# Kernel optimization log

Hardware: AMD Instinct MI355X
Metric: run time of the kernel (lower is better)

## Reference

```python
import jax, jax.numpy as jnp
import numpy as np

N_USERS = 100000
N_ITEMS = 50000
EMB_DIM = 64
N_LAYERS = 2
N_INTENTS = 128
N_EDGES = 4000000
N_NODES = N_USERS + N_ITEMS


def setup_inputs() -> dict:
    key = jax.random.key(0)
    k1, k2, k3, k4, k5 = jax.random.split(key, 5)
    return {
        "user_emb": 0.1 * jax.random.normal(k1, (N_USERS, EMB_DIM), dtype=jnp.float32),
        "item_emb": 0.1 * jax.random.normal(k2, (N_ITEMS, EMB_DIM), dtype=jnp.float32),
        "intents": jax.random.normal(k3, (EMB_DIM, N_INTENTS), dtype=jnp.float32) * (2.0 / (EMB_DIM + N_INTENTS)) ** 0.5,
        "h_idx": jax.random.randint(k4, (N_EDGES,), 0, N_NODES, dtype=jnp.int64)
        if jax.config.jax_enable_x64 else jax.random.randint(k4, (N_EDGES,), 0, N_NODES, dtype=jnp.int32),
        "t_idx": jax.random.randint(k5, (N_EDGES,), 0, N_NODES, dtype=jnp.int32),
    }


def _spmm(h_idx, t_idx, g_vals, x):
    # y[h] += g_vals * x[t]  (sparse matrix @ dense, COO form)
    gathered = x[t_idx] * g_vals[:, None]  # [E, D]
    return jax.ops.segment_sum(gathered, h_idx, num_segments=N_NODES)


def reference(user_emb, item_emb, intents, h_idx, t_idx):
    # --- _cal_sparse_adj: G = D^{-1/2} A D^{-1/2}, A values are ones ---
    deg = jax.ops.segment_sum(jnp.ones_like(h_idx, dtype=user_emb.dtype), h_idx,
                              num_segments=N_NODES)
    d_inv_sqrt = jnp.where(deg > 0, jax.lax.rsqrt(jnp.maximum(deg, 1e-12)), 0.0)
    g_vals = d_inv_sqrt[h_idx] * d_inv_sqrt[t_idx]  # [E]

    # --- multi-layer propagation with intent-aware embeddings ---
    embs = jnp.concatenate([user_emb, item_emb], axis=0)  # [N, D]
    all_embs = [embs]
    for _ in range(N_LAYERS):
        gnn_embs = _spmm(h_idx, t_idx, g_vals, embs)  # [N, D]
        # intent projection: softmax over intents, reconstruct in emb space
        u, it = embs[:N_USERS], embs[N_USERS:]
        u_int = jax.nn.softmax(u @ intents, axis=1) @ intents.T      # [n_users, D]
        i_int = jax.nn.softmax(it @ intents, axis=1) @ intents.T     # [n_items, D]
        int_embs = jnp.concatenate([u_int, i_int], axis=0)
        embs = gnn_embs + int_embs
        all_embs.append(embs)
    out = jnp.sum(jnp.stack(all_embs, axis=1), axis=1) / len(all_embs)  # mean over layers
    return out
```

## Files before the change

kernel.cpp:

```cpp
#include <hip/hip_runtime.h>
#include <math.h>

#define N_USERS 100000
#define N_ITEMS 50000
#define N_NODES 150000
#define EMB 64
#define NI 128
#define NUM_EDGES 4000000
#define NPAD 150016
#define NB 586
#define BSTRIDE 8192
#define ETILE 8192
#define EGRID ((NUM_EDGES + ETILE - 1) / ETILE)
#define NTILES (N_NODES / 16)
#define SBLK ((NTILES + 3) / 4)

typedef __attribute__((ext_vector_type(8))) short bf16x8;
typedef __attribute__((ext_vector_type(4))) float f32x4;

__device__ __forceinline__ unsigned short f2bf(float f) {
    unsigned int u = __float_as_uint(f);
    u += 0x7FFFu + ((u >> 16) & 1u);
    return (unsigned short)(u >> 16);
}
__device__ __forceinline__ float bflo(unsigned int u) { return __uint_as_float(u << 16); }
__device__ __forceinline__ float bfhi(unsigned int u) { return __uint_as_float(u & 0xFFFF0000u); }
__device__ __forceinline__ int cl_idx(unsigned int v) {
    int x = (int)(v & 0x3FFFFu);
    return (x < N_NODES) ? x : (N_NODES - 1);
}


__global__ __launch_bounds__(512) void bucket_scatter(const int* __restrict__ h,
                                                      const int* __restrict__ t,
                                                      int* __restrict__ gcur,
                                                      unsigned int* __restrict__ ebuf) {
    __shared__ int lc[NB];
    __shared__ int lbase[NB];
    __shared__ int lcur[NB];
    int tid = threadIdx.x;
    for (int i = tid; i < NB; i += 512) lc[i] = 0;
    __syncthreads();
    int base = blockIdx.x * ETILE;
#pragma unroll
    for (int k = 0; k < ETILE / 512; ++k) {
        int idx = base + k * 512 + tid;
        if (idx < NUM_EDGES) atomicAdd(&lc[h[idx] >> 8], 1);
    }
    __syncthreads();
    for (int i = tid; i < NB; i += 512) {
        int c = lc[i];
        lbase[i] = c ? (i * BSTRIDE + atomicAdd(&gcur[i], c)) : 0;
        lcur[i] = 0;
    }
    __syncthreads();
#pragma unroll
    for (int k = 0; k < ETILE / 512; ++k) {
        int idx = base + k * 512 + tid;
        if (idx < NUM_EDGES) {
            int hh = h[idx], tt = t[idx];
            int b = hh >> 8;
            int p = lbase[b] + atomicAdd(&lcur[b], 1);
            int lim = b * BSTRIDE + BSTRIDE - 1;
            p = (p <= lim) ? p : lim;
            ebuf[p] = ((unsigned int)(hh & 255) << 18) | (unsigned int)tt;
        }
    }
}


__global__ __launch_bounds__(512) void bucket_csr(const int* __restrict__ gcur,
                                                  unsigned int* __restrict__ ebuf,
                                                  int2* __restrict__ rmeta,
                                                  float* __restrict__ dinv) {
    __shared__ unsigned int in_s[BSTRIDE];
    __shared__ int cnt_s[256];
    __shared__ int base_s[256];
    __shared__ int sc[256];
    int b = blockIdx.x, tid = threadIdx.x;
    int s = b * BSTRIDE;
    int n = gcur[b];
    if (n > BSTRIDE) n = BSTRIDE;

    for (int i = tid; i < n; i += 512) in_s[i] = ebuf[s + i];
    if (tid < 256) cnt_s[tid] = 0;
    __syncthreads();
    for (int i = tid; i < n; i += 512) atomicAdd(&cnt_s[in_s[i] >> 18], 1);
    __syncthreads();

    int c = 0;
    if (tid < 256) { c = cnt_s[tid]; sc[tid] = c; }
    __syncthreads();
    for (int off = 1; off < 256; off <<= 1) {
        int tv = 0;
        if (tid < 256 && tid >= off) tv = sc[tid - off];
        __syncthreads();
        if (tid < 256 && tid >= off) sc[tid] += tv;
        __syncthreads();
    }
    if (tid < 256) {
        int excl = sc[tid] - c;
        base_s[tid] = excl;
        int node = (b << 8) + tid;
        rmeta[node] = make_int2(s + excl, c);
        dinv[node] = (c > 0) ? rsqrtf((float)c) : 0.0f;
        cnt_s[tid] = 0;
    }
    __syncthreads();

    for (int i = tid; i < n; i += 512) {
        unsigned int qv = in_s[i];
        int hl = (int)(qv >> 18);
        int p = base_s[hl] + atomicAdd(&cnt_s[hl], 1);
        ebuf[s + p] = qv & 0x3FFFFu;
    }
}


__global__ void init_kernel(const float4* __restrict__ ue4, const float4* __restrict__ ie4,
                            uint2* __restrict__ ebf4, float4* __restrict__ out4) {
    int i = blockIdx.x * blockDim.x + threadIdx.x;
    const int uelems = N_USERS * EMB / 4;
    const int total  = N_NODES * EMB / 4;
    if (i < total) {
        float4 v = (i < uelems) ? ue4[i] : ie4[i - uelems];
        out4[i] = v;
        unsigned int p0 = ((unsigned int)f2bf(v.y) << 16) | f2bf(v.x);
        unsigned int p1 = ((unsigned int)f2bf(v.w) << 16) | f2bf(v.z);
        ebf4[i] = make_uint2(p0, p1);
    }
}


__global__ __launch_bounds__(256) void wconv(const float* __restrict__ W,
                                             unsigned short* __restrict__ Wt,
                                             unsigned short* __restrict__ W2b) {
    int i = blockIdx.x * 256 + threadIdx.x;
    if (i < EMB * NI) {
        int d = i >> 7, c = i & 127;
        unsigned short b = f2bf(W[i]);
        W2b[i] = b;
        Wt[c * EMB + d] = b;
    }
}


__global__ __launch_bounds__(256, 6) void spmm_intent(const int2* __restrict__ rmeta,
                                                      const unsigned int* __restrict__ col,
                                                      const float* __restrict__ dinv,
                                                      const unsigned short* __restrict__ ebf,
                                                      unsigned short* __restrict__ ebfout,
                                                      const unsigned short* __restrict__ Wt,
                                                      const unsigned short* __restrict__ W2b,
                                                      float* __restrict__ acc, float scale) {
    __shared__ __align__(16) float UPool[4][1408];

    int tid = threadIdx.x;
    int wid = tid >> 6, lane = tid & 63;
    int q = lane >> 4, c = lane & 15;
    int qq = lane >> 3, cc = lane & 7;
    int tile = blockIdx.x * 4 + wid;
    if (tile >= NTILES) return;
    int rowbase = tile << 4;
    float* fw = &UPool[wid][0];
    unsigned short* pw = (unsigned short*)&UPool[wid][1088];

#pragma unroll 1
    for (int half = 0; half < 2; ++half) {
        int row = rowbase + half * 8 + qq;
        int2 rm = rmeta[row];
        int s = rm.x, deg = rm.y;
        float dr = dinv[row];
        int dm = deg;
        dm = max(dm, __shfl_xor(dm, 8));
        dm = max(dm, __shfl_xor(dm, 16));
        dm = max(dm, __shfl_xor(dm, 32));
        dm = __builtin_amdgcn_readfirstlane(dm);

        float a0 = 0.f, a1 = 0.f, a2 = 0.f, a3 = 0.f;
        float a4 = 0.f, a5 = 0.f, a6 = 0.f, a7 = 0.f;
        int last = s + ((deg > 0) ? (deg - 1) : 0);
        const unsigned short* eb = ebf + (cc << 3);

        int ce0 = cl_idx(col[s]);
        int ce1 = cl_idx(col[min(s + 1, last)]);
        int ce2 = cl_idx(col[min(s + 2, last)]);
        int ce3 = cl_idx(col[min(s + 3, last)]);
        float g0 = dinv[ce0], g1 = dinv[ce1], g2 = dinv[ce2], g3 = dinv[ce3];
        uint4 u0 = *(const uint4*)(eb + ((size_t)ce0 << 6));
        uint4 u1 = *(const uint4*)(eb + ((size_t)ce1 << 6));
        uint4 u2 = *(const uint4*)(eb + ((size_t)ce2 << 6));
        uint4 u3 = *(const uint4*)(eb + ((size_t)ce3 << 6));
        int nc0 = cl_idx(col[min(s + 4, last)]);
        int nc1 = cl_idx(col[min(s + 5, last)]);
        int nc2 = cl_idx(col[min(s + 6, last)]);
        int nc3 = cl_idx(col[min(s + 7, last)]);

        for (int it = 0; it < dm; it += 4) {
            int f0 = cl_idx(col[min(s + it + 8, last)]);
            int f1 = cl_idx(col[min(s + it + 9, last)]);
            int f2 = cl_idx(col[min(s + it + 10, last)]);
            int f3 = cl_idx(col[min(s + it + 11, last)]);
            float h0 = dinv[nc0], h1 = dinv[nc1], h2 = dinv[nc2], h3 = dinv[nc3];
            uint4 v0 = *(const uint4*)(eb + ((size_t)nc0 << 6));
            uint4 v1 = *(const uint4*)(eb + ((size_t)nc1 << 6));
            uint4 v2 = *(const uint4*)(eb + ((size_t)nc2 << 6));
            uint4 v3 = *(const uint4*)(eb + ((size_t)nc3 << 6));
            float gu0 = (it     < deg) ? g0 : 0.f;
            float gu1 = (it + 1 < deg) ? g1 : 0.f;
            float gu2 = (it + 2 < deg) ? g2 : 0.f;
            float gu3 = (it + 3 < deg) ? g3 : 0.f;
            a0 = fmaf(gu0, bflo(u0.x), a0); a1 = fmaf(gu0, bfhi(u0.x), a1);
            a2 = fmaf(gu0, bflo(u0.y), a2); a3 = fmaf(gu0, bfhi(u0.y), a3);
            a4 = fmaf(gu0, bflo(u0.z), a4); a5 = fmaf(gu0, bfhi(u0.z), a5);
            a6 = fmaf(gu0, bflo(u0.w), a6); a7 = fmaf(gu0, bfhi(u0.w), a7);
            a0 = fmaf(gu1, bflo(u1.x), a0); a1 = fmaf(gu1, bfhi(u1.x), a1);
            a2 = fmaf(gu1, bflo(u1.y), a2); a3 = fmaf(gu1, bfhi(u1.y), a3);
            a4 = fmaf(gu1, bflo(u1.z), a4); a5 = fmaf(gu1, bfhi(u1.z), a5);
            a6 = fmaf(gu1, bflo(u1.w), a6); a7 = fmaf(gu1, bfhi(u1.w), a7);
            a0 = fmaf(gu2, bflo(u2.x), a0); a1 = fmaf(gu2, bfhi(u2.x), a1);
            a2 = fmaf(gu2, bflo(u2.y), a2); a3 = fmaf(gu2, bfhi(u2.y), a3);
            a4 = fmaf(gu2, bflo(u2.z), a4); a5 = fmaf(gu2, bfhi(u2.z), a5);
            a6 = fmaf(gu2, bflo(u2.w), a6); a7 = fmaf(gu2, bfhi(u2.w), a7);
            a0 = fmaf(gu3, bflo(u3.x), a0); a1 = fmaf(gu3, bfhi(u3.x), a1);
            a2 = fmaf(gu3, bflo(u3.y), a2); a3 = fmaf(gu3, bfhi(u3.y), a3);
            a4 = fmaf(gu3, bflo(u3.z), a4); a5 = fmaf(gu3, bfhi(u3.z), a5);
            a6 = fmaf(gu3, bflo(u3.w), a6); a7 = fmaf(gu3, bfhi(u3.w), a7);
            u0 = v0; u1 = v1; u2 = v2; u3 = v3;
            g0 = h0; g1 = h1; g2 = h2; g3 = h3;
            nc0 = f0; nc1 = f1; nc2 = f2; nc3 = f3;
        }
        int fb = (half * 8 + qq) * 68 + (cc << 3);
        fw[fb + 0] = a0 * dr; fw[fb + 1] = a1 * dr;
        fw[fb + 2] = a2 * dr; fw[fb + 3] = a3 * dr;
        fw[fb + 4] = a4 * dr; fw[fb + 5] = a5 * dr;
        fw[fb + 6] = a6 * dr; fw[fb + 7] = a7 * dr;
    }

    const unsigned short* erow = ebf + ((size_t)(rowbase + c) << 6);
    bf16x8 A0 = *(const bf16x8*)(erow + (q << 3));
    bf16x8 A1 = *(const bf16x8*)(erow + 32 + (q << 3));
    f32x4 S[8];
#pragma unroll
    for (int t = 0; t < 8; ++t) {
        bf16x8 B0 = *(const bf16x8*)&Wt[(16 * t + c) * EMB + (q << 3)];
        bf16x8 B1 = *(const bf16x8*)&Wt[(16 * t + c) * EMB + 32 + (q << 3)];
        f32x4 z = {0.f, 0.f, 0.f, 0.f};
        z = __builtin_amdgcn_mfma_f32_16x16x32_bf16(A0, B0, z, 0, 0, 0);
        S[t] = __builtin_amdgcn_mfma_f32_16x16x32_bf16(A1, B1, z, 0, 0, 0);
    }

#pragma unroll
    for (int r = 0; r < 4; ++r) {
        float m = S[0][r];
#pragma unroll
        for (int t = 1; t < 8; ++t) m = fmaxf(m, S[t][r]);
        m = fmaxf(m, __shfl_xor(m, 1)); m = fmaxf(m, __shfl_xor(m, 2));
        m = fmaxf(m, __shfl_xor(m, 4)); m = fmaxf(m, __shfl_xor(m, 8));
        float sum = 0.f;
#pragma unroll
        for (int t = 0; t < 8; ++t) { float ex = __expf(S[t][r] - m); S[t][r] = ex; sum += ex; }
        sum += __shfl_xor(sum, 1); sum += __shfl_xor(sum, 2);
        sum += __shfl_xor(sum, 4); sum += __shfl_xor(sum, 8);
        float inv = 1.0f / sum;
#pragma unroll
        for (int t = 0; t < 8; ++t) S[t][r] *= inv;
    }

    f32x4 O0 = {0.f, 0.f, 0.f, 0.f}, O1 = O0, O2 = O0, O3 = O0;
#pragma unroll
    for (int s2 = 0; s2 < 4; ++s2) {
#pragma unroll
        for (int h2 = 0; h2 < 2; ++h2) {
            int t = 2 * s2 + h2;
#pragma unroll
            for (int r = 0; r < 4; ++r) {
                float p = S[t][r];
                unsigned short b = f2bf(p);
                pw[(4 * q + r) * 40 + (h2 << 4) + c] = b;
                S[t][r] = p - bflo((unsigned int)b);
            }
        }
        bf16x8 Pf = *(const bf16x8*)&pw[c * 40 + (q << 3)];
        {
            bf16x8 Bf0 = *(const bf16x8*)&W2b[(c) * NI + (s2 << 5) + (q << 3)];
            bf16x8 Bf1 = *(const bf16x8*)&W2b[(16 + c) * NI + (s2 << 5) + (q << 3)];
            O0 = __builtin_amdgcn_mfma_f32_16x16x32_bf16(Pf, Bf0, O0, 0, 0, 0);
            O1 = __builtin_amdgcn_mfma_f32_16x16x32_bf16(Pf, Bf1, O1, 0, 0, 0);
            bf16x8 Bf2 = *(const bf16x8*)&W2b[(32 + c) * NI + (s2 << 5) + (q << 3)];
            bf16x8 Bf3 = *(const bf16x8*)&W2b[(48 + c) * NI + (s2 << 5) + (q << 3)];
            O2 = __builtin_amdgcn_mfma_f32_16x16x32_bf16(Pf, Bf2, O2, 0, 0, 0);
            O3 = __builtin_amdgcn_mfma_f32_16x16x32_bf16(Pf, Bf3, O3, 0, 0, 0);
        }
#pragma unroll
        for (int h2 = 0; h2 < 2; ++h2) {
            int t = 2 * s2 + h2;
#pragma unroll
            for (int r = 0; r < 4; ++r)
                pw[(4 * q + r) * 40 + (h2 << 4) + c] = f2bf(S[t][r]);
        }
        bf16x8 Pl = *(const bf16x8*)&pw[c * 40 + (q << 3)];
        {
            bf16x8 Bf0 = *(const bf16x8*)&W2b[(c) * NI + (s2 << 5) + (q << 3)];
            bf16x8 Bf1 = *(const bf16x8*)&W2b[(16 + c) * NI + (s2 << 5) + (q << 3)];
            O0 = __builtin_amdgcn_mfma_f32_16x16x32_bf16(Pl, Bf0, O0, 0, 0, 0);
            O1 = __builtin_amdgcn_mfma_f32_16x16x32_bf16(Pl, Bf1, O1, 0, 0, 0);
            bf16x8 Bf2 = *(const bf16x8*)&W2b[(32 + c) * NI + (s2 << 5) + (q << 3)];
            bf16x8 Bf3 = *(const bf16x8*)&W2b[(48 + c) * NI + (s2 << 5) + (q << 3)];
            O2 = __builtin_amdgcn_mfma_f32_16x16x32_bf16(Pl, Bf2, O2, 0, 0, 0);
            O3 = __builtin_amdgcn_mfma_f32_16x16x32_bf16(Pl, Bf3, O3, 0, 0, 0);
        }
    }

    asm volatile("" ::: "memory");

#pragma unroll
    for (int r = 0; r < 4; ++r) {
        int rl = 4 * q + r;
        float* gr = &fw[rl * 68];
        gr[c]      += O0[r];
        gr[16 + c] += O1[r];
        gr[32 + c] += O2[r];
        gr[48 + c] += O3[r];
    }

    {
        int j = lane >> 2, sg = lane & 3;
        const float* gr = &fw[j * 68 + (sg << 4)];
        float4 x0 = *(const float4*)&gr[0];
        float4 x1 = *(const float4*)&gr[4];
        float4 x2 = *(const float4*)&gr[8];
        float4 x3 = *(const float4*)&gr[12];
        size_t base = ((size_t)(rowbase + j) << 6) + (sg << 4);
        uint4 w0, w1;
        w0.x = (unsigned int)f2bf(x0.x) | ((unsigned int)f2bf(x0.y) << 16);
        w0.y = (unsigned int)f2bf(x0.z) | ((unsigned int)f2bf(x0.w) << 16);
        w0.z = (unsigned int)f2bf(x1.x) | ((unsigned int)f2bf(x1.y) << 16);
        w0.w = (unsigned int)f2bf(x1.z) | ((unsigned int)f2bf(x1.w) << 16);
        w1.x = (unsigned int)f2bf(x2.x) | ((unsigned int)f2bf(x2.y) << 16);
        w1.y = (unsigned int)f2bf(x2.z) | ((unsigned int)f2bf(x2.w) << 16);
        w1.z = (unsigned int)f2bf(x3.x) | ((unsigned int)f2bf(x3.y) << 16);
        w1.w = (unsigned int)f2bf(x3.z) | ((unsigned int)f2bf(x3.w) << 16);
        *(uint4*)(ebfout + base) = w0;
        *(uint4*)(ebfout + base + 8) = w1;
        float4* ap = (float4*)(acc + base);
        float4 b0 = ap[0], b1 = ap[1], b2 = ap[2], b3 = ap[3];
        b0.x = (b0.x + x0.x) * scale; b0.y = (b0.y + x0.y) * scale;
        b0.z = (b0.z + x0.z) * scale; b0.w = (b0.w + x0.w) * scale;
        b1.x = (b1.x + x1.x) * scale; b1.y = (b1.y + x1.y) * scale;
        b1.z = (b1.z + x1.z) * scale; b1.w = (b1.w + x1.w) * scale;
        b2.x = (b2.x + x2.x) * scale; b2.y = (b2.y + x2.y) * scale;
        b2.z = (b2.z + x2.z) * scale; b2.w = (b2.w + x2.w) * scale;
        b3.x = (b3.x + x3.x) * scale; b3.y = (b3.y + x3.y) * scale;
        b3.z = (b3.z + x3.z) * scale; b3.w = (b3.w + x3.w) * scale;
        ap[0] = b0; ap[1] = b1; ap[2] = b2; ap[3] = b3;
    }
}


extern "C" void kernel_launch(void* const* d_in, const int* in_sizes, int n_in,
                              void* d_out, int out_size, void* d_ws, size_t ws_size,
                              hipStream_t stream) {
    const float* ue = (const float*)d_in[0];
    const float* ie = (const float*)d_in[1];
    const float* W  = (const float*)d_in[2];
    const int*   h  = (const int*)d_in[3];
    const int*   t  = (const int*)d_in[4];
    float* out = (float*)d_out;

    int*            gcur  = (int*)d_ws;
    int2*           rmeta = (int2*)(gcur + 1024);
    float*          dinv  = (float*)(rmeta + NPAD);
    unsigned int*   ebuf  = (unsigned int*)(dinv + NPAD);
    unsigned short* Wt    = (unsigned short*)(ebuf + NB * BSTRIDE);
    unsigned short* W2b   = Wt + EMB * NI;
    unsigned short* ebfA  = W2b + EMB * NI;
    unsigned short* ebfB  = ebfA + (size_t)NPAD * EMB;

    hipMemsetAsync(gcur, 0, NB * sizeof(int), stream);
    bucket_scatter<<<EGRID, 512, 0, stream>>>(h, t, gcur, ebuf);
    bucket_csr<<<NB, 512, 0, stream>>>(gcur, ebuf, rmeta, dinv);
    init_kernel<<<(N_NODES * EMB / 4 + 255) / 256, 256, 0, stream>>>(
        (const float4*)ue, (const float4*)ie, (uint2*)ebfA, (float4*)out);
    wconv<<<(EMB * NI + 255) / 256, 256, 0, stream>>>(W, Wt, W2b);

    const unsigned int* col = ebuf;
    spmm_intent<<<SBLK, 256, 0, stream>>>(rmeta, col, dinv, ebfA, ebfB, Wt, W2b, out, 1.0f);
    spmm_intent<<<SBLK, 256, 0, stream>>>(rmeta, col, dinv, ebfB, ebfA, Wt, W2b, out, 1.0f / 3.0f);
}
```

Before: 453.2 us.

## Sort rows by degree within buckets and pad row lengths with sentinel edges

The CSR build now pads each row's edge list to a multiple of four using a sentinel column that points at a zeroed padding node, and it produces a per-bucket permutation that orders nodes by descending degree. The SpMM kernel processes rows in permuted order, so the eight rows sharing a wavefront have similar degrees. This removes the per-edge bounds clamps, the degree masks and the wavefront max-degree reduction. Occupancy hint raised from 6 to 7. Risks: a bucket can overflow BSTRIDE once padding is added, and rows are written in scattered permuted order.

```diff
diff --git a/kernel.cpp b/kernel.cpp
--- a/kernel.cpp
+++ b/kernel.cpp
@@ -12,8 +12,9 @@
 #define BSTRIDE 8192
 #define ETILE 8192
 #define EGRID ((NUM_EDGES + ETILE - 1) / ETILE)
-#define NTILES (N_NODES / 16)
-#define SBLK ((NTILES + 3) / 4)
+#define NT_ALL (NPAD / 16)
+#define SBLK (NT_ALL / 4)
+#define SENT 150000u
 
 typedef __attribute__((ext_vector_type(8))) short bf16x8;
 typedef __attribute__((ext_vector_type(4))) float f32x4;
@@ -25,10 +26,6 @@
 }
 __device__ __forceinline__ float bflo(unsigned int u) { return __uint_as_float(u << 16); }
 __device__ __forceinline__ float bfhi(unsigned int u) { return __uint_as_float(u & 0xFFFF0000u); }
-__device__ __forceinline__ int cl_idx(unsigned int v) {
-    int x = (int)(v & 0x3FFFFu);
-    return (x < N_NODES) ? x : (N_NODES - 1);
-}
 
 
 __global__ __launch_bounds__(512) void bucket_scatter(const int* __restrict__ h,
@@ -72,24 +69,33 @@
 __global__ __launch_bounds__(512) void bucket_csr(const int* __restrict__ gcur,
                                                   unsigned int* __restrict__ ebuf,
                                                   int2* __restrict__ rmeta,
-                                                  float* __restrict__ dinv) {
+                                                  float* __restrict__ dinv,
+                                                  int* __restrict__ perm) {
     __shared__ unsigned int in_s[BSTRIDE];
     __shared__ int cnt_s[256];
     __shared__ int base_s[256];
     __shared__ int sc[256];
+    __shared__ int dh[256];
+    __shared__ int dcur[256];
     int b = blockIdx.x, tid = threadIdx.x;
     int s = b * BSTRIDE;
     int n = gcur[b];
     if (n > BSTRIDE) n = BSTRIDE;
 
     for (int i = tid; i < n; i += 512) in_s[i] = ebuf[s + i];
-    if (tid < 256) cnt_s[tid] = 0;
+    if (tid < 256) { cnt_s[tid] = 0; dh[tid] = 0; dcur[tid] = 0; }
     __syncthreads();
     for (int i = tid; i < n; i += 512) atomicAdd(&cnt_s[in_s[i] >> 18], 1);
     __syncthreads();
 
-    int c = 0;
-    if (tid < 256) { c = cnt_s[tid]; sc[tid] = c; }
+    int c = 0, pc = 0, key = 0;
+    if (tid < 256) {
+        c = cnt_s[tid];
+        pc = (c + 3) & ~3;
+        sc[tid] = pc;
+        key = 255 - min(c, 255);
+        atomicAdd(&dh[key], 1);
+    }
     __syncthreads();
     for (int off = 1; off < 256; off <<= 1) {
         int tv = 0;
@@ -98,16 +104,28 @@
         if (tid < 256 && tid >= off) sc[tid] += tv;
         __syncthreads();
     }
+    int excl = 0;
+    if (tid < 256) { excl = sc[tid] - pc; base_s[tid] = excl; }
+    __syncthreads();
+    if (tid < 256) sc[tid] = dh[tid];
+    __syncthreads();
+    for (int off = 1; off < 256; off <<= 1) {
+        int tv = 0;
+        if (tid < 256 && tid >= off) tv = sc[tid - off];
+        __syncthreads();
+        if (tid < 256 && tid >= off) sc[tid] += tv;
+        __syncthreads();
+    }
     if (tid < 256) {
-        int excl = sc[tid] - c;
-        base_s[tid] = excl;
         int node = (b << 8) + tid;
-        rmeta[node] = make_int2(s + excl, c);
+        rmeta[node] = make_int2(s + excl, pc);
         dinv[node] = (c > 0) ? rsqrtf((float)c) : 0.0f;
+        int pos = (sc[key] - dh[key]) + atomicAdd(&dcur[key], 1);
+        perm[(b << 8) + pos] = node;
+        for (int p2 = c; p2 < pc; ++p2) ebuf[s + excl + p2] = SENT;
         cnt_s[tid] = 0;
     }
     __syncthreads();
-
     for (int i = tid; i < n; i += 512) {
         unsigned int qv = in_s[i];
         int hl = (int)(qv >> 18);
@@ -121,10 +139,13 @@
                             uint2* __restrict__ ebf4, float4* __restrict__ out4) {
     int i = blockIdx.x * blockDim.x + threadIdx.x;
     const int uelems = N_USERS * EMB / 4;
-    const int total  = N_NODES * EMB / 4;
+    const int relems = N_NODES * EMB / 4;
+    const int total  = NPAD * EMB / 4;
     if (i < total) {
-        float4 v = (i < uelems) ? ue4[i] : ie4[i - uelems];
-        out4[i] = v;
+        float4 v = make_float4(0.f, 0.f, 0.f, 0.f);
+        if (i < uelems) v = ue4[i];
+        else if (i < relems) v = ie4[i - uelems];
+        if (i < relems) out4[i] = v;
         unsigned int p0 = ((unsigned int)f2bf(v.y) << 16) | f2bf(v.x);
         unsigned int p1 = ((unsigned int)f2bf(v.w) << 16) | f2bf(v.z);
         ebf4[i] = make_uint2(p0, p1);
@@ -145,9 +166,10 @@
 }
 
 
-__global__ __launch_bounds__(256, 6) void spmm_intent(const int2* __restrict__ rmeta,
+__global__ __launch_bounds__(256, 7) void spmm_intent(const int2* __restrict__ rmeta,
                                                       const unsigned int* __restrict__ col,
                                                       const float* __restrict__ dinv,
+                                                      const int* __restrict__ perm,
                                                       const unsigned short* __restrict__ ebf,
                                                       unsigned short* __restrict__ ebfout,
                                                       const unsigned short* __restrict__ Wt,
@@ -160,75 +182,65 @@
     int q = lane >> 4, c = lane & 15;
     int qq = lane >> 3, cc = lane & 7;
     int tile = blockIdx.x * 4 + wid;
-    if (tile >= NTILES) return;
+    if (tile >= NT_ALL) return;
     int rowbase = tile << 4;
     float* fw = &UPool[wid][0];
     unsigned short* pw = (unsigned short*)&UPool[wid][1088];
 
 #pragma unroll 1
     for (int half = 0; half < 2; ++half) {
-        int row = rowbase + half * 8 + qq;
-        int2 rm = rmeta[row];
-        int s = rm.x, deg = rm.y;
-        float dr = dinv[row];
-        int dm = deg;
-        dm = max(dm, __shfl_xor(dm, 8));
-        dm = max(dm, __shfl_xor(dm, 16));
-        dm = max(dm, __shfl_xor(dm, 32));
-        dm = __builtin_amdgcn_readfirstlane(dm);
+        int prow = perm[rowbase + half * 8 + qq];
+        int2 rm = rmeta[prow];
+        int s = rm.x, pcv = rm.y;
+        float dr = dinv[prow];
 
         float a0 = 0.f, a1 = 0.f, a2 = 0.f, a3 = 0.f;
         float a4 = 0.f, a5 = 0.f, a6 = 0.f, a7 = 0.f;
-        int last = s + ((deg > 0) ? (deg - 1) : 0);
         const unsigned short* eb = ebf + (cc << 3);
 
-        int ce0 = cl_idx(col[s]);
-        int ce1 = cl_idx(col[min(s + 1, last)]);
-        int ce2 = cl_idx(col[min(s + 2, last)]);
-        int ce3 = cl_idx(col[min(s + 3, last)]);
-        float g0 = dinv[ce0], g1 = dinv[ce1], g2 = dinv[ce2], g3 = dinv[ce3];
-        uint4 u0 = *(const uint4*)(eb + ((size_t)ce0 << 6));
-        uint4 u1 = *(const uint4*)(eb + ((size_t)ce1 << 6));
-        uint4 u2 = *(const uint4*)(eb + ((size_t)ce2 << 6));
-        uint4 u3 = *(const uint4*)(eb + ((size_t)ce3 << 6));
-        int nc0 = cl_idx(col[min(s + 4, last)]);
-        int nc1 = cl_idx(col[min(s + 5, last)]);
-        int nc2 = cl_idx(col[min(s + 6, last)]);
-        int nc3 = cl_idx(col[min(s + 7, last)]);
-
-        for (int it = 0; it < dm; it += 4) {
-            int f0 = cl_idx(col[min(s + it + 8, last)]);
-            int f1 = cl_idx(col[min(s + it + 9, last)]);
-            int f2 = cl_idx(col[min(s + it + 10, last)]);
-            int f3 = cl_idx(col[min(s + it + 11, last)]);
-            float h0 = dinv[nc0], h1 = dinv[nc1], h2 = dinv[nc2], h3 = dinv[nc3];
-            uint4 v0 = *(const uint4*)(eb + ((size_t)nc0 << 6));
-            uint4 v1 = *(const uint4*)(eb + ((size_t)nc1 << 6));
-            uint4 v2 = *(const uint4*)(eb + ((size_t)nc2 << 6));
-            uint4 v3 = *(const uint4*)(eb + ((size_t)nc3 << 6));
-            float gu0 = (it     < deg) ? g0 : 0.f;
-            float gu1 = (it + 1 < deg) ? g1 : 0.f;
-            float gu2 = (it + 2 < deg) ? g2 : 0.f;
-            float gu3 = (it + 3 < deg) ? g3 : 0.f;
-            a0 = fmaf(gu0, bflo(u0.x), a0); a1 = fmaf(gu0, bfhi(u0.x), a1);
-            a2 = fmaf(gu0, bflo(u0.y), a2); a3 = fmaf(gu0, bfhi(u0.y), a3);
-            a4 = fmaf(gu0, bflo(u0.z), a4); a5 = fmaf(gu0, bfhi(u0.z), a5);
-            a6 = fmaf(gu0, bflo(u0.w), a6); a7 = fmaf(gu0, bfhi(u0.w), a7);
-            a0 = fmaf(gu1, bflo(u1.x), a0); a1 = fmaf(gu1, bfhi(u1.x), a1);
-            a2 = fmaf(gu1, bflo(u1.y), a2); a3 = fmaf(gu1, bfhi(u1.y), a3);
-            a4 = fmaf(gu1, bflo(u1.z), a4); a5 = fmaf(gu1, bfhi(u1.z), a5);
-            a6 = fmaf(gu1, bflo(u1.w), a6); a7 = fmaf(gu1, bfhi(u1.w), a7);
-            a0 = fmaf(gu2, bflo(u2.x), a0); a1 = fmaf(gu2, bfhi(u2.x), a1);
-            a2 = fmaf(gu2, bflo(u2.y), a2); a3 = fmaf(gu2, bfhi(u2.y), a3);
-            a4 = fmaf(gu2, bflo(u2.z), a4); a5 = fmaf(gu2, bfhi(u2.z), a5);
-            a6 = fmaf(gu2, bflo(u2.w), a6); a7 = fmaf(gu2, bfhi(u2.w), a7);
-            a0 = fmaf(gu3, bflo(u3.x), a0); a1 = fmaf(gu3, bfhi(u3.x), a1);
-            a2 = fmaf(gu3, bflo(u3.y), a2); a3 = fmaf(gu3, bfhi(u3.y), a3);
-            a4 = fmaf(gu3, bflo(u3.z), a4); a5 = fmaf(gu3, bfhi(u3.z), a5);
-            a6 = fmaf(gu3, bflo(u3.w), a6); a7 = fmaf(gu3, bfhi(u3.w), a7);
+        int e0 = (int)(col[s]     & 0x3FFFFu);
+        int e1 = (int)(col[s + 1] & 0x3FFFFu);
+        int e2 = (int)(col[s + 2] & 0x3FFFFu);
+        int e3 = (int)(col[s + 3] & 0x3FFFFu);
+        float g0 = dinv[e0], g1 = dinv[e1], g2 = dinv[e2], g3 = dinv[e3];
+        uint4 u0 = *(const uint4*)(eb + ((size_t)e0 << 6));
+        uint4 u1 = *(const uint4*)(eb + ((size_t)e1 << 6));
+        uint4 u2 = *(const uint4*)(eb + ((size_t)e2 << 6));
+        uint4 u3 = *(const uint4*)(eb + ((size_t)e3 << 6));
+        int f0 = (int)(col[s + 4] & 0x3FFFFu);
+        int f1 = (int)(col[s + 5] & 0x3FFFFu);
+        int f2 = (int)(col[s + 6] & 0x3FFFFu);
+        int f3 = (int)(col[s + 7] & 0x3FFFFu);
+
+        for (int it = 0; it < pcv; it += 4) {
+            float h0 = dinv[f0], h1 = dinv[f1], h2 = dinv[f2], h3 = dinv[f3];
+            uint4 v0 = *(const uint4*)(eb + ((size_t)f0 << 6));
+            uint4 v1 = *(const uint4*)(eb + ((size_t)f1 << 6));
+            uint4 v2 = *(const uint4*)(eb + ((size_t)f2 << 6));
+            uint4 v3 = *(const uint4*)(eb + ((size_t)f3 << 6));
+            int x0 = (int)(col[s + it + 8]  & 0x3FFFFu);
+            int x1 = (int)(col[s + it + 9]  & 0x3FFFFu);
+            int x2 = (int)(col[s + it + 10] & 0x3FFFFu);
+            int x3 = (int)(col[s + it + 11] & 0x3FFFFu);
+            a0 = fmaf(g0, bflo(u0.x), a0); a1 = fmaf(g0, bfhi(u0.x), a1);
+            a2 = fmaf(g0, bflo(u0.y), a2); a3 = fmaf(g0, bfhi(u0.y), a3);
+            a4 = fmaf(g0, bflo(u0.z), a4); a5 = fmaf(g0, bfhi(u0.z), a5);
+            a6 = fmaf(g0, bflo(u0.w), a6); a7 = fmaf(g0, bfhi(u0.w), a7);
+            a0 = fmaf(g1, bflo(u1.x), a0); a1 = fmaf(g1, bfhi(u1.x), a1);
+            a2 = fmaf(g1, bflo(u1.y), a2); a3 = fmaf(g1, bfhi(u1.y), a3);
+            a4 = fmaf(g1, bflo(u1.z), a4); a5 = fmaf(g1, bfhi(u1.z), a5);
+            a6 = fmaf(g1, bflo(u1.w), a6); a7 = fmaf(g1, bfhi(u1.w), a7);
+            a0 = fmaf(g2, bflo(u2.x), a0); a1 = fmaf(g2, bfhi(u2.x), a1);
+            a2 = fmaf(g2, bflo(u2.y), a2); a3 = fmaf(g2, bfhi(u2.y), a3);
+            a4 = fmaf(g2, bflo(u2.z), a4); a5 = fmaf(g2, bfhi(u2.z), a5);
+            a6 = fmaf(g2, bflo(u2.w), a6); a7 = fmaf(g2, bfhi(u2.w), a7);
+            a0 = fmaf(g3, bflo(u3.x), a0); a1 = fmaf(g3, bfhi(u3.x), a1);
+            a2 = fmaf(g3, bflo(u3.y), a2); a3 = fmaf(g3, bfhi(u3.y), a3);
+            a4 = fmaf(g3, bflo(u3.z), a4); a5 = fmaf(g3, bfhi(u3.z), a5);
+            a6 = fmaf(g3, bflo(u3.w), a6); a7 = fmaf(g3, bfhi(u3.w), a7);
             u0 = v0; u1 = v1; u2 = v2; u3 = v3;
             g0 = h0; g1 = h1; g2 = h2; g3 = h3;
-            nc0 = f0; nc1 = f1; nc2 = f2; nc3 = f3;
+            f0 = x0; f1 = x1; f2 = x2; f3 = x3;
         }
         int fb = (half * 8 + qq) * 68 + (cc << 3);
         fw[fb + 0] = a0 * dr; fw[fb + 1] = a1 * dr;
@@ -237,7 +249,8 @@
         fw[fb + 6] = a6 * dr; fw[fb + 7] = a7 * dr;
     }
 
-    const unsigned short* erow = ebf + ((size_t)(rowbase + c) << 6);
+    int arow = perm[rowbase + c];
+    const unsigned short* erow = ebf + ((size_t)arow << 6);
     bf16x8 A0 = *(const bf16x8*)(erow + (q << 3));
     bf16x8 A1 = *(const bf16x8*)(erow + 32 + (q << 3));
     f32x4 S[8];
@@ -326,12 +339,13 @@
 
     {
         int j = lane >> 2, sg = lane & 3;
+        int rw = perm[rowbase + j];
         const float* gr = &fw[j * 68 + (sg << 4)];
         float4 x0 = *(const float4*)&gr[0];
         float4 x1 = *(const float4*)&gr[4];
         float4 x2 = *(const float4*)&gr[8];
         float4 x3 = *(const float4*)&gr[12];
-        size_t base = ((size_t)(rowbase + j) << 6) + (sg << 4);
+        size_t base = ((size_t)rw << 6) + (sg << 4);
         uint4 w0, w1;
         w0.x = (unsigned int)f2bf(x0.x) | ((unsigned int)f2bf(x0.y) << 16);
         w0.y = (unsigned int)f2bf(x0.z) | ((unsigned int)f2bf(x0.w) << 16);
@@ -343,17 +357,19 @@
         w1.w = (unsigned int)f2bf(x3.z) | ((unsigned int)f2bf(x3.w) << 16);
         *(uint4*)(ebfout + base) = w0;
         *(uint4*)(ebfout + base + 8) = w1;
-        float4* ap = (float4*)(acc + base);
-        float4 b0 = ap[0], b1 = ap[1], b2 = ap[2], b3 = ap[3];
-        b0.x = (b0.x + x0.x) * scale; b0.y = (b0.y + x0.y) * scale;
-        b0.z = (b0.z + x0.z) * scale; b0.w = (b0.w + x0.w) * scale;
-        b1.x = (b1.x + x1.x) * scale; b1.y = (b1.y + x1.y) * scale;
-        b1.z = (b1.z + x1.z) * scale; b1.w = (b1.w + x1.w) * scale;
-        b2.x = (b2.x + x2.x) * scale; b2.y = (b2.y + x2.y) * scale;
-        b2.z = (b2.z + x2.z) * scale; b2.w = (b2.w + x2.w) * scale;
-        b3.x = (b3.x + x3.x) * scale; b3.y = (b3.y + x3.y) * scale;
-        b3.z = (b3.z + x3.z) * scale; b3.w = (b3.w + x3.w) * scale;
-        ap[0] = b0; ap[1] = b1; ap[2] = b2; ap[3] = b3;
+        if (rw < N_NODES) {
+            float4* ap = (float4*)(acc + base);
+            float4 b0 = ap[0], b1 = ap[1], b2 = ap[2], b3 = ap[3];
+            b0.x = (b0.x + x0.x) * scale; b0.y = (b0.y + x0.y) * scale;
+            b0.z = (b0.z + x0.z) * scale; b0.w = (b0.w + x0.w) * scale;
+            b1.x = (b1.x + x1.x) * scale; b1.y = (b1.y + x1.y) * scale;
+            b1.z = (b1.z + x1.z) * scale; b1.w = (b1.w + x1.w) * scale;
+            b2.x = (b2.x + x2.x) * scale; b2.y = (b2.y + x2.y) * scale;
+            b2.z = (b2.z + x2.z) * scale; b2.w = (b2.w + x2.w) * scale;
+            b3.x = (b3.x + x3.x) * scale; b3.y = (b3.y + x3.y) * scale;
+            b3.z = (b3.z + x3.z) * scale; b3.w = (b3.w + x3.w) * scale;
+            ap[0] = b0; ap[1] = b1; ap[2] = b2; ap[3] = b3;
+        }
     }
 }
 
@@ -371,20 +387,22 @@
     int*            gcur  = (int*)d_ws;
     int2*           rmeta = (int2*)(gcur + 1024);
     float*          dinv  = (float*)(rmeta + NPAD);
-    unsigned int*   ebuf  = (unsigned int*)(dinv + NPAD);
-    unsigned short* Wt    = (unsigned short*)(ebuf + NB * BSTRIDE);
+    int*            perm  = (int*)(dinv + NPAD);
+    unsigned short* ebfA  = (unsigned short*)(perm + NPAD);
+    unsigned short* ebfB  = ebfA + (size_t)NPAD * EMB;
+    unsigned int*   ebuf  = (unsigned int*)(ebfB + (size_t)NPAD * EMB);
+    unsigned short* Wt    = (unsigned short*)(ebuf + NB * BSTRIDE + 16);
     unsigned short* W2b   = Wt + EMB * NI;
-    unsigned short* ebfA  = W2b + EMB * NI;
-    unsigned short* ebfB  = ebfA + (size_t)NPAD * EMB;
 
     hipMemsetAsync(gcur, 0, NB * sizeof(int), stream);
+    hipMemsetAsync(ebuf + NB * BSTRIDE, 0, 16 * sizeof(unsigned int), stream);
     bucket_scatter<<<EGRID, 512, 0, stream>>>(h, t, gcur, ebuf);
-    bucket_csr<<<NB, 512, 0, stream>>>(gcur, ebuf, rmeta, dinv);
-    init_kernel<<<(N_NODES * EMB / 4 + 255) / 256, 256, 0, stream>>>(
+    bucket_csr<<<NB, 512, 0, stream>>>(gcur, ebuf, rmeta, dinv, perm);
+    init_kernel<<<(NPAD * EMB / 4 + 255) / 256, 256, 0, stream>>>(
         (const float4*)ue, (const float4*)ie, (uint2*)ebfA, (float4*)out);
     wconv<<<(EMB * NI + 255) / 256, 256, 0, stream>>>(W, Wt, W2b);
 
     const unsigned int* col = ebuf;
-    spmm_intent<<<SBLK, 256, 0, stream>>>(rmeta, col, dinv, ebfA, ebfB, Wt, W2b, out, 1.0f);
-    spmm_intent<<<SBLK, 256, 0, stream>>>(rmeta, col, dinv, ebfB, ebfA, Wt, W2b, out, 1.0f / 3.0f);
-}
+    spmm_intent<<<SBLK, 256, 0, stream>>>(rmeta, col, dinv, perm, ebfA, ebfB, Wt, W2b, out, 1.0f);
+    spmm_intent<<<SBLK, 256, 0, stream>>>(rmeta, col, dinv, perm, ebfB, ebfA, Wt, W2b, out, 1.0f / 3.0f);
+}
```

Measured after the change: 488.0 us. +7.7%, slower.
